# Optimization experiments

Hardware: AMD Instinct MI355X
Metric: run time of the kernel (lower is better)

## Reference

```python
import jax, jax.numpy as jnp
import numpy as np

NUM_HEADS = 8
NUM_LAYERS = 4
TOKEN_AMOUNT = 16
TOKEN_SIZE = 256
D_MODEL = 512
D_FF = 2048


def _layernorm(x, g, b, eps=1e-6):
    m = jnp.mean(x, axis=-1, keepdims=True)
    v = jnp.mean((x - m) ** 2, axis=-1, keepdims=True)
    return (x - m) / jnp.sqrt(v + eps) * g + b


def _mha(xq, xkv, W, b, mask, H):
    # W: [4, d, d] (q,k,v,o), b: [4, d]
    B, Tq, d = xq.shape
    Tk = xkv.shape[1]
    dh = d // H
    q = (xq @ W[0] + b[0]).reshape(B, Tq, H, dh).transpose(0, 2, 1, 3)
    k = (xkv @ W[1] + b[1]).reshape(B, Tk, H, dh).transpose(0, 2, 1, 3)
    v = (xkv @ W[2] + b[2]).reshape(B, Tk, H, dh).transpose(0, 2, 1, 3)
    logits = jnp.einsum('bhqd,bhkd->bhqk', q, k) / jnp.sqrt(jnp.float32(dh))
    if mask is not None:
        logits = logits - mask * jnp.finfo(jnp.float32).max
    w = jax.nn.softmax(logits, axis=-1)
    o = jnp.einsum('bhqk,bhkd->bhqd', w, v).transpose(0, 2, 1, 3).reshape(B, Tq, d)
    return o @ W[3] + b[3]


def _pos_enc(T, d):
    i = jnp.arange(d)
    factors = 1.0 / jnp.power(10000.0, (2.0 * (i // 2)).astype(jnp.float32) / d)
    ang = jnp.arange(T, dtype=jnp.float32)[:, None] * factors  # [T, d]
    return jnp.where(i % 2 == 0, jnp.sin(ang), jnp.cos(ang))


def setup_inputs() -> dict:
    key = jax.random.key(0)
    ks = jax.random.split(key, 8)
    B, Lenc, F = 16, 2048, 128
    d, dff, L, TS = D_MODEL, D_FF, NUM_LAYERS, TOKEN_SIZE
    s = 0.02
    return {
        'encoder_output': jax.random.normal(ks[0], (B, Lenc, d), jnp.float32),
        'encoder_input': jax.random.normal(ks[1], (B, Lenc, F), jnp.float32),
        'emb_W': jax.random.normal(ks[2], (TS, d), jnp.float32) * s,
        'emb_b': jnp.zeros((d,), jnp.float32),
        'out_W': jax.random.normal(ks[3], (d, TS), jnp.float32) * s,
        'out_b': jnp.zeros((TS,), jnp.float32),
        'self_W': jax.random.normal(ks[4], (L, 4, d, d), jnp.float32) * s,
        'self_b': jnp.zeros((L, 4, d), jnp.float32),
        'cross_W': jax.random.normal(ks[5], (L, 4, d, d), jnp.float32) * s,
        'cross_b': jnp.zeros((L, 4, d), jnp.float32),
        'ffn_W1': jax.random.normal(ks[6], (L, d, dff), jnp.float32) * s,
        'ffn_b1': jnp.zeros((L, dff), jnp.float32),
        'ffn_W2': jax.random.normal(ks[7], (L, dff, d), jnp.float32) * s,
        'ffn_b2': jnp.zeros((L, d), jnp.float32),
        'ln_g': jnp.ones((L, 3, d), jnp.float32),
        'ln_b': jnp.zeros((L, 3, d), jnp.float32),
    }


def reference(encoder_output, encoder_input, emb_W, emb_b, out_W, out_b,
              self_W, self_b, cross_W, cross_b,
              ffn_W1, ffn_b1, ffn_W2, ffn_b2, ln_g, ln_b):
    B = encoder_output.shape[0]
    d = emb_W.shape[1]
    H = NUM_HEADS
    # padding mask from encoder_input (mask_zero_inputs=True)
    pad_mask = jnp.min((encoder_input == 0).astype(jnp.float32), axis=2)[:, None, None, :]
    tokens = jnp.ones((B, 1, TOKEN_SIZE), dtype=jnp.float32)
    for _ in range(TOKEN_AMOUNT):
        T = tokens.shape[1]
        look_ahead = 1.0 - jnp.tril(jnp.ones((T, T), dtype=jnp.float32))
        tok_pad = jnp.min((tokens == 0).astype(jnp.float32), axis=2)[:, None, None, :]
        la_mask = jnp.maximum(tok_pad, look_ahead)
        x = (tokens @ emb_W + emb_b) * jnp.sqrt(jnp.float32(d)) + _pos_enc(T, d)
        for l in range(NUM_LAYERS):
            a = _mha(x, x, self_W[l], self_b[l], la_mask, H)
            x = _layernorm(x + a, ln_g[l, 0], ln_b[l, 0])
            c = _mha(x, encoder_output, cross_W[l], cross_b[l], pad_mask, H)
            x = _layernorm(x + c, ln_g[l, 1], ln_b[l, 1])
            f = jax.nn.relu(x @ ffn_W1[l] + ffn_b1[l]) @ ffn_W2[l] + ffn_b2[l]
            x = _layernorm(x + f, ln_g[l, 2], ln_b[l, 2])
        next_token = (x @ out_W + out_b)[:, -1:, :]
        tokens = jnp.concatenate([tokens, next_token], axis=1)
    return tokens[:, 1:, :]
```

## Files before the change

### kernel.cpp

```cpp
#include <hip/hip_runtime.h>


typedef unsigned short ushort_t;
typedef __attribute__((ext_vector_type(4))) float f32x4;
typedef __attribute__((ext_vector_type(8))) unsigned short us8;
typedef __attribute__((ext_vector_type(4))) unsigned short us4;

#define NB 256
#define NTHR 1024

__device__ __forceinline__ float bf2f(ushort_t u) {
    union { unsigned int i; float f; } v; v.i = ((unsigned int)u) << 16; return v.f;
}
__device__ __forceinline__ ushort_t f2bf(float f) {
    union { unsigned int i; float f; } v; v.f = f;
    return (ushort_t)((v.i + 0x7FFF + ((v.i >> 16) & 1)) >> 16);
}
__device__ __forceinline__ f32x4 b2f4(us4 w) {
    return (f32x4){bf2f(w[0]), bf2f(w[1]), bf2f(w[2]), bf2f(w[3])};
}
__device__ __forceinline__ float wave_sum(float v) {
    #pragma unroll
    for (int m = 32; m; m >>= 1) v += __shfl_xor(v, m);
    return v;
}
__device__ __forceinline__ float wave_max(float v) {
    #pragma unroll
    for (int m = 32; m; m >>= 1) v = fmaxf(v, __shfl_xor(v, m));
    return v;
}

union U64C { unsigned long long u; float2 f; us4 s4; };
__device__ __forceinline__ float clf(const float* p) {
    return __hip_atomic_load(p, __ATOMIC_RELAXED, __HIP_MEMORY_SCOPE_AGENT);
}
__device__ __forceinline__ void csf(float* p, float v) {
    __hip_atomic_store(p, v, __ATOMIC_RELAXED, __HIP_MEMORY_SCOPE_AGENT);
}
__device__ __forceinline__ float2 clf2(const float* p) {
    U64C c; c.u = __hip_atomic_load((unsigned long long*)p, __ATOMIC_RELAXED,
                                    __HIP_MEMORY_SCOPE_AGENT);
    return c.f;
}
__device__ __forceinline__ void csf2(float* p, float x, float y) {
    U64C c; c.f.x = x; c.f.y = y;
    __hip_atomic_store((unsigned long long*)p, c.u, __ATOMIC_RELAXED,
                       __HIP_MEMORY_SCOPE_AGENT);
}
__device__ __forceinline__ void csu4(ushort_t* p, us4 v) {
    U64C c; c.s4 = v;
    __hip_atomic_store((unsigned long long*)p, c.u, __ATOMIC_RELAXED,
                       __HIP_MEMORY_SCOPE_AGENT);
}

__device__ __forceinline__ void gbar(unsigned* bar, int g) {
    __syncthreads();
    if (threadIdx.x == 0) {
        unsigned* cnt = bar + g * 32;
        unsigned* rel = bar + 512 + g * 32;
        unsigned a = __hip_atomic_fetch_add(cnt, 1u, __ATOMIC_RELAXED,
                                            __HIP_MEMORY_SCOPE_AGENT);
        unsigned e = (a >> 4) + 1u;
        if ((a & 15u) == 15u) {
            __hip_atomic_store(rel, e, __ATOMIC_RELAXED, __HIP_MEMORY_SCOPE_AGENT);
        } else {
            while ((int)(__hip_atomic_load(rel, __ATOMIC_RELAXED,
                                           __HIP_MEMORY_SCOPE_AGENT) - e) < 0)
                __builtin_amdgcn_s_sleep(1);
        }
    }
    __syncthreads();
}
__device__ __forceinline__ void gbar_all(unsigned* bar) {
    __syncthreads();
    if (threadIdx.x == 0) {
        unsigned* cnt = bar + 1024;
        unsigned* rel = bar + 1056;
        unsigned a = __hip_atomic_fetch_add(cnt, 1u, __ATOMIC_RELAXED,
                                            __HIP_MEMORY_SCOPE_AGENT);
        unsigned e = (a >> 8) + 1u;
        if ((a & 255u) == 255u) {
            __hip_atomic_store(rel, e, __ATOMIC_RELAXED, __HIP_MEMORY_SCOPE_AGENT);
        } else {
            while ((int)(__hip_atomic_load(rel, __ATOMIC_RELAXED,
                                           __HIP_MEMORY_SCOPE_AGENT) - e) < 0)
                __builtin_amdgcn_s_sleep(1);
        }
    }
    __syncthreads();
}

__device__ __forceinline__ void ln512b(const float* __restrict__ row,
                                       const float* __restrict__ g,
                                       const float* __restrict__ be,
                                       int use_ln, float* dst, float* red) {
    int tid = threadIdx.x;
    float a = (tid < 512) ? clf(row + tid) : 0.f;
    if (use_ln) {
        float s = a, s2 = a * a;
        #pragma unroll
        for (int m = 32; m; m >>= 1) {
            s  += __shfl_xor(s, m);
            s2 += __shfl_xor(s2, m);
        }
        if ((tid & 63) == 0) { red[tid >> 6] = s; red[16 + (tid >> 6)] = s2; }
        __syncthreads();
        float ts = 0.f, ts2 = 0.f;
        #pragma unroll
        for (int i = 0; i < 8; i++) { ts += red[i]; ts2 += red[16 + i]; }
        float mu = ts * (1.f / 512.f);
        float var = ts2 * (1.f / 512.f) - mu * mu;
        float rstd = rsqrtf(var + 1e-6f);
        if (tid < 512) dst[tid] = (a - mu) * rstd * g[tid] + be[tid];
    } else {
        if (tid < 512) dst[tid] = a;
    }
    __syncthreads();
}

template<int NCQ, int K>
__device__ __forceinline__ void gemv_allf(const float* xs, const float* __restrict__ W,
                                          int ldw, int col0, float* part) {
    constexpr int S = 1024 / NCQ;
    constexpr int KS = K / S;
    int tid = threadIdx.x;
    int cq = tid & (NCQ - 1), ks = tid / NCQ;
    const float* Wp = W + (size_t)(ks * KS) * ldw + col0 + cq * 4;
    const float* xp = xs + ks * KS;
    f32x4 acc = {0.f, 0.f, 0.f, 0.f};
    #pragma unroll
    for (int r = 0; r < KS; r++)
        acc += xp[r] * *(const f32x4*)(Wp + (size_t)r * ldw);
    #pragma unroll
    for (int m = NCQ; m < 64; m <<= 1) {
        acc[0] += __shfl_xor(acc[0], m);
        acc[1] += __shfl_xor(acc[1], m);
        acc[2] += __shfl_xor(acc[2], m);
        acc[3] += __shfl_xor(acc[3], m);
    }
    int wave = tid >> 6, lane = tid & 63;
    if (lane < NCQ) *(f32x4*)(part + (wave * NCQ + lane) * 4) = acc;
    __syncthreads();
}

template<int NCQ, int K>
__device__ __forceinline__ void gemv_allb(const float* xs, const ushort_t* __restrict__ W,
                                          int ldw, int col0, float* part) {
    constexpr int S = 1024 / NCQ;
    constexpr int KS = K / S;
    int tid = threadIdx.x;
    int cq = tid & (NCQ - 1), ks = tid / NCQ;
    const ushort_t* Wp = W + (size_t)(ks * KS) * ldw + col0 + cq * 4;
    const float* xp = xs + ks * KS;
    f32x4 acc = {0.f, 0.f, 0.f, 0.f};
    #pragma unroll
    for (int r = 0; r < KS; r++)
        acc += xp[r] * b2f4(*(const us4*)(Wp + (size_t)r * ldw));
    #pragma unroll
    for (int m = NCQ; m < 64; m <<= 1) {
        acc[0] += __shfl_xor(acc[0], m);
        acc[1] += __shfl_xor(acc[1], m);
        acc[2] += __shfl_xor(acc[2], m);
        acc[3] += __shfl_xor(acc[3], m);
    }
    int wave = tid >> 6, lane = tid & 63;
    if (lane < NCQ) *(f32x4*)(part + (wave * NCQ + lane) * 4) = acc;
    __syncthreads();
}
template<int NCQ>
__device__ __forceinline__ float gemv_allr(const float* part) {
    float a = 0.f;
    #pragma unroll
    for (int w = 0; w < 16; w++) a += part[w * NCQ * 4 + threadIdx.x];
    return a;
}

struct Args {
    const float *enc, *encIn, *embW, *embB, *outW, *outB;
    const float *selfW, *selfB, *crossW, *crossB;
    const float *fW1, *fb1, *fW2, *fb2, *lng, *lnb;
    float* out;
    unsigned* bar;
    float *x0, *qbuf, *y1, *y2, *y3, *attnb;
    float *lny1, *lny2, *qt, *Pm2, *Ps2, *Pz, *tmpb, *selfK, *selfV;
    ushort_t *selfWb, *crossWb, *fW1b, *fW2b;
};


__global__ __launch_bounds__(NTHR, 4) void k_mega(Args A) {
    __shared__ ushort_t encL[128 * 520];
    __shared__ float padL[128];
    __shared__ float sm[6400];
    const int bid = blockIdx.x, tid = threadIdx.x;
    const int b = bid >> 4, r = bid & 15;
    unsigned* bar = A.bar;

    {
        const float* ep = A.enc + ((size_t)b * 2048 + r * 128) * 512;
        #pragma unroll 4
        for (int it = 0; it < 16; it++) {
            int idx = tid + it * 1024;
            int key = idx >> 7;
            int d = (idx & 127) * 4;
            float4 v = *(const float4*)(ep + (size_t)key * 512 + d);
            us4 o; o[0] = f2bf(v.x); o[1] = f2bf(v.y); o[2] = f2bf(v.z); o[3] = f2bf(v.w);
            *(us4*)(encL + key * 520 + d) = o;
        }
        int key = tid >> 3, sub = tid & 7;
        const float* p = A.encIn + ((size_t)b * 2048 + r * 128 + key) * 128 + sub * 16;
        int ok = 1;
        #pragma unroll
        for (int j = 0; j < 4; j++) {
            float4 v = *(const float4*)(p + j * 4);
            ok &= (v.x == 0.f) & (v.y == 0.f) & (v.z == 0.f) & (v.w == 0.f);
        }
        ok &= __shfl_xor(ok, 1); ok &= __shfl_xor(ok, 2); ok &= __shfl_xor(ok, 4);
        if (sub == 0) padL[key] = ok ? 1.f : 0.f;
        const float* srcs[4] = {A.selfW, A.crossW, A.fW1, A.fW2};
        ushort_t* dsts[4] = {A.selfWb, A.crossWb, A.fW1b, A.fW2b};
        #pragma unroll
        for (int a = 0; a < 4; a++) {
            const float* s = srcs[a];
            ushort_t* d = dsts[a];
            #pragma unroll
            for (int it = 0; it < 4; it++) {
                size_t i = (size_t)bid * 16384 + (size_t)(it * 1024 + tid) * 4;
                float4 v = *(const float4*)(s + i);
                us4 o; o[0] = f2bf(v.x); o[1] = f2bf(v.y); o[2] = f2bf(v.z); o[3] = f2bf(v.w);
                csu4(d + i, o);
            }
        }
    }
    gbar_all(bar);

    for (int t = 0; t < 16; t++) {
        {
            float* tok = sm;
            float* part = sm + 256;
            if (tid < 256)
                tok[tid] = (t == 0) ? 1.f
                         : clf(A.out + (size_t)b * 4096 + (t - 1) * 256 + tid);
            __syncthreads();
            gemv_allf<8, 256>(tok, A.embW, 512, r * 32, part);
            if (tid < 32) {
                float acc = gemv_allr<8>(part);
                int col = r * 32 + tid;
                float expo = (2.0f * (float)(col >> 1)) * (1.f / 512.f);
                float ang = (float)t * powf(10000.0f, -expo);
                float pv = (col & 1) ? cosf(ang) : sinf(ang);
                csf(A.x0 + (size_t)b * 512 + col,
                    (acc + A.embB[col]) * 22.627416997969522f + pv);
            }
        }
        gbar(bar, b);

        for (int l = 0; l < 4; l++) {
            const float* src = (l == 0) ? A.x0 : A.y3;
            const float* gP = (l == 0) ? nullptr : A.lng + ((l - 1) * 3 + 2) * 512;
            const float* bP = (l == 0) ? nullptr : A.lnb + ((l - 1) * 3 + 2) * 512;
            int ulnP = (l != 0);

            {
                float* xs = sm;
                float* red = sm + 512;
                float* part = sm + 1024;
                ln512b(src + (size_t)b * 512, gP, bP, ulnP, xs, red);
                int cq = tid & 7, ks = tid >> 3;
                const float* xp = xs + ks * 4;
                f32x4 a0 = {0.f,0.f,0.f,0.f}, a1 = a0, a2 = a0;
                const ushort_t* W0 = A.selfWb + ((size_t)(l * 4 + 0)) * 262144
                                   + (size_t)(ks * 4) * 512 + r * 32 + cq * 4;
                const ushort_t* W1 = W0 + 262144;
                const ushort_t* W2 = W1 + 262144;
                #pragma unroll
                for (int rr = 0; rr < 4; rr++) {
                    float x = xp[rr];
                    a0 += x * b2f4(*(const us4*)(W0 + (size_t)rr * 512));
                    a1 += x * b2f4(*(const us4*)(W1 + (size_t)rr * 512));
                    a2 += x * b2f4(*(const us4*)(W2 + (size_t)rr * 512));
                }
                #pragma unroll
                for (int m = 8; m < 64; m <<= 1) {
                    #pragma unroll
                    for (int j = 0; j < 4; j++) {
                        a0[j] += __shfl_xor(a0[j], m);
                        a1[j] += __shfl_xor(a1[j], m);
                        a2[j] += __shfl_xor(a2[j], m);
                    }
                }
                int wave = tid >> 6, lane = tid & 63;
                if (lane < 8) {
                    *(f32x4*)(part + (wave * 8 + lane) * 4) = a0;
                    *(f32x4*)(part + 512 + (wave * 8 + lane) * 4) = a1;
                    *(f32x4*)(part + 1024 + (wave * 8 + lane) * 4) = a2;
                }
                __syncthreads();
                if (tid < 96) {
                    int m = tid >> 5, j = tid & 31;
                    float a = 0.f;
                    #pragma unroll
                    for (int w = 0; w < 16; w++) a += part[m * 512 + w * 32 + j];
                    int col = r * 32 + j;
                    a += A.selfB[(l * 4 + m) * 512 + col];
                    if (m == 0) csf(A.qbuf + (size_t)b * 512 + col, a);
                    else if (m == 1)
                        csf(A.selfK + (((size_t)l * 16 + b) * 16 + t) * 512 + col, a);
                    else
                        csf(A.selfV + (((size_t)l * 16 + b) * 16 + t) * 512 + col, a);
                }
            }
            gbar(bar, b);

            {
                float* xr = sm;
                float* qs = sm + 512;
                float* as2 = sm + 1024;
                float* lg = sm + 5120;
                float* red = sm + 5248;
                float* part = sm + 5280;
                ln512b(src + (size_t)b * 512, gP, bP, ulnP, xr, red);
                if (tid < 256) {
                    float2 v = clf2(A.qbuf + (size_t)b * 512 + tid * 2);
                    qs[tid * 2] = v.x; qs[tid * 2 + 1] = v.y;
                }
                __syncthreads();
                const float* Kb = A.selfK + ((size_t)l * 16 + b) * 16 * 512;
                const float* Vb = A.selfV + ((size_t)l * 16 + b) * 16 * 512;
                {
                    int idx = tid >> 3, kp = tid & 7;
                    int h = idx >> 4, j = idx & 15;
                    if (j <= t) {
                        const float* kpp = Kb + (size_t)j * 512 + h * 64 + kp * 8;
                        const float* qp = qs + h * 64 + kp * 8;
                        float4 k0 = *(const float4*)kpp;
                        float4 k1 = *(const float4*)(kpp + 4);
                        float s = qp[0]*k0.x + qp[1]*k0.y + qp[2]*k0.z + qp[3]*k0.w
                                + qp[4]*k1.x + qp[5]*k1.y + qp[6]*k1.z + qp[7]*k1.w;
                        s += __shfl_xor(s, 1);
                        s += __shfl_xor(s, 2);
                        s += __shfl_xor(s, 4);
                        if (kp == 0) lg[h * 16 + j] = s * 0.125f;
                    }
                }
                __syncthreads();
                if (tid < 8) {
                    float m = -1e30f;
                    for (int j = 0; j <= t; j++) m = fmaxf(m, lg[tid * 16 + j]);
                    float ssum = 0.f;
                    for (int j = 0; j <= t; j++) {
                        float e = __expf(lg[tid * 16 + j] - m);
                        lg[tid * 16 + j] = e; ssum += e;
                    }
                    float inv = 1.f / ssum;
                    for (int j = 0; j <= t; j++) lg[tid * 16 + j] *= inv;
                }
                __syncthreads();
                {
                    int cq2 = tid & 127, js = tid >> 7;
                    int col0 = cq2 * 4, h = col0 >> 6;
                    f32x4 acc = {0.f, 0.f, 0.f, 0.f};
                    for (int j = js; j <= t; j += 8) {
                        float4 v = *(const float4*)(Vb + (size_t)j * 512 + col0);
                        float w = lg[h * 16 + j];
                        acc[0] += w * v.x; acc[1] += w * v.y;
                        acc[2] += w * v.z; acc[3] += w * v.w;
                    }
                    *(f32x4*)(as2 + js * 512 + col0) = acc;
                }
                __syncthreads();
                if (tid < 512) {
                    float a = 0.f;
                    #pragma unroll
                    for (int s = 0; s < 8; s++) a += as2[s * 512 + tid];
                    qs[tid] = a;
                }
                __syncthreads();
                gemv_allb<8, 512>(qs, A.selfWb + ((size_t)(l * 4 + 3)) * 262144,
                                  512, r * 32, part);
                if (tid < 32) {
                    int col = r * 32 + tid;
                    csf(A.y1 + (size_t)b * 512 + col,
                        gemv_allr<8>(part) + A.selfB[(l * 4 + 3) * 512 + col] + xr[col]);
                }
            }
            gbar(bar, b);

            {
                int h = r >> 1, half = r & 1;
                float* xsw = sm;
                float* red = sm + 512;
                float* qch = sm + 544;
                float* part = sm + 1024;
                ln512b(A.y1 + (size_t)b * 512, A.lng + (l * 3) * 512,
                       A.lnb + (l * 3) * 512, 1, xsw, red);
                if (r == 0 && tid < 512)
                    csf(A.lny1 + (size_t)b * 512 + tid, xsw[tid]);
                gemv_allb<16, 512>(xsw, A.crossWb + ((size_t)(l * 4)) * 262144,
                                   512, h * 64, part);
                if (tid < 64)
                    qch[tid] = gemv_allr<16>(part)
                             + A.crossB[(l * 4) * 512 + h * 64 + tid];
                __syncthreads();
                {
                    int D = half * 256 + (tid >> 2), q4 = tid & 3;
                    const ushort_t* wr = A.crossWb + ((size_t)(l * 4 + 1)) * 262144
                                       + (size_t)D * 512 + h * 64 + q4 * 16;
                    const float* qp = qch + q4 * 16;
                    float a = 0.f;
                    #pragma unroll
                    for (int j = 0; j < 16; j += 4) {
                        f32x4 wv = b2f4(*(const us4*)(wr + j));
                        a += qp[j]*wv[0] + qp[j+1]*wv[1] + qp[j+2]*wv[2] + qp[j+3]*wv[3];
                    }
                    a += __shfl_xor(a, 1);
                    a += __shfl_xor(a, 2);
                    if (q4 == 0)
                        csf(A.qt + ((size_t)b * 8 + h) * 512 + D, a * 0.125f);
                }
            }
            gbar(bar, b);

            {
                float* qts = sm;
                float* lge = sm + 4160;
                float* wms = sm + 5184;
                float* wss = sm + 5200;
                #pragma unroll
                for (int it = 0; it < 2; it++) {
                    int p = (tid + it * 1024) * 2;
                    float2 v = clf2(A.qt + (size_t)b * 4096 + p);
                    int row = p >> 9, d = p & 511;
                    qts[row * 520 + d] = v.x;
                    qts[row * 520 + d + 1] = v.y;
                }
                __syncthreads();
                #pragma unroll
                for (int it = 0; it < 4; it++) {
                    int key = it * 32 + (tid >> 5);
                    int hh = (tid >> 2) & 7, pq = tid & 3;
                    const ushort_t* er = encL + key * 520;
                    const float* q = qts + hh * 520;
                    float a0 = 0.f, a1 = 0.f;
                    #pragma unroll
                    for (int ch = 0; ch < 16; ch++) {
                        int c8 = (pq + ch * 4) * 8;
                        us8 ev8 = *(const us8*)(er + c8);
                        const float* qp = q + c8;
                        a0 += bf2f(ev8[0])*qp[0] + bf2f(ev8[1])*qp[1]
                            + bf2f(ev8[2])*qp[2] + bf2f(ev8[3])*qp[3];
                        a1 += bf2f(ev8[4])*qp[4] + bf2f(ev8[5])*qp[5]
                            + bf2f(ev8[6])*qp[6] + bf2f(ev8[7])*qp[7];
                    }
                    float acc = a0 + a1;
                    acc += __shfl_xor(acc, 1);
                    acc += __shfl_xor(acc, 2);
                    if (pq == 0)
                        lge[hh * 128 + key] = (padL[key] != 0.f) ? -2e30f : acc;
                }
                __syncthreads();
                {
                    int hh = tid >> 7, k = tid & 127;
                    float lv = lge[hh * 128 + k];
                    float mv = wave_max(lv);
                    if ((tid & 63) == 0) wms[tid >> 6] = mv;
                    __syncthreads();
                    float m = fmaxf(wms[hh * 2], wms[hh * 2 + 1]);
                    float ev = __expf(lv - m);
                    float sv = wave_sum(ev);
                    if ((tid & 63) == 0) wss[tid >> 6] = sv;
                    lge[hh * 128 + k] = ev;
                    __syncthreads();
                    if (tid < 8) {
                        int bc = b * 16 + r;
                        csf(A.Pm2 + bc * 8 + tid, fmaxf(wms[tid * 2], wms[tid * 2 + 1]));
                        csf(A.Ps2 + bc * 8 + tid, wss[tid * 2] + wss[tid * 2 + 1]);
                    }
                }
                __syncthreads();
                {
                    int hz = tid >> 7, ii = tid & 127;
                    f32x4 z = {0.f, 0.f, 0.f, 0.f};
                    const ushort_t* ep2 = encL + ii * 4;
                    const float* le = lge + hz * 128;
                    #pragma unroll 4
                    for (int k = 0; k < 128; k++) {
                        float ev = le[k];
                        us4 e4 = *(const us4*)(ep2 + k * 520);
                        z[0] += ev * bf2f(e4[0]); z[1] += ev * bf2f(e4[1]);
                        z[2] += ev * bf2f(e4[2]); z[3] += ev * bf2f(e4[3]);
                    }
                    float* dst = A.Pz + ((size_t)((b * 16 + r) * 8 + hz)) * 512 + ii * 4;
                    csf2(dst, z[0], z[1]);
                    csf2(dst + 2, z[2], z[3]);
                }
            }
            gbar(bar, b);

            {
                int h = r >> 1, half = r & 1;
                float* zs = sm;
                float* zs2 = sm + 512;
                float* ecs = sm + 2560;
                float* part = sm + 2624;
                if (tid < 16) {
                    float mcv = clf(A.Pm2 + (b * 16 + tid) * 8 + h);
                    float mm = mcv;
                    mm = fmaxf(mm, __shfl_xor(mm, 1));
                    mm = fmaxf(mm, __shfl_xor(mm, 2));
                    mm = fmaxf(mm, __shfl_xor(mm, 4));
                    mm = fmaxf(mm, __shfl_xor(mm, 8));
                    float ec = __expf(mcv - mm);
                    float sv = ec * clf(A.Ps2 + (b * 16 + tid) * 8 + h);
                    sv += __shfl_xor(sv, 1); sv += __shfl_xor(sv, 2);
                    sv += __shfl_xor(sv, 4); sv += __shfl_xor(sv, 8);
                    ecs[tid] = ec;
                    if (tid == 0) ecs[16] = 1.f / sv;
                }
                __syncthreads();
                {
                    int cp = (tid & 255) * 2, qtr = tid >> 8;
                    float a0 = 0.f, a1 = 0.f;
                    #pragma unroll
                    for (int j = 0; j < 4; j++) {
                        int cc = qtr * 4 + j;
                        float2 v = clf2(A.Pz + ((size_t)(b * 16 + cc) * 8 + h) * 512 + cp);
                        a0 += ecs[cc] * v.x; a1 += ecs[cc] * v.y;
                    }
                    zs2[qtr * 512 + cp] = a0;
                    zs2[qtr * 512 + cp + 1] = a1;
                }
                __syncthreads();
                if (tid < 512)
                    zs[tid] = (zs2[tid] + zs2[512 + tid] + zs2[1024 + tid]
                             + zs2[1536 + tid]) * ecs[16];
                __syncthreads();
                gemv_allb<8, 512>(zs, A.crossWb + ((size_t)(l * 4 + 2)) * 262144,
                                  512, h * 64 + half * 32, part);
                if (tid < 32) {
                    int col = h * 64 + half * 32 + tid;
                    csf(A.attnb + (size_t)b * 512 + col,
                        gemv_allr<8>(part) + A.crossB[(l * 4 + 2) * 512 + col]);
                }
            }
            gbar(bar, b);

            {
                float* xa = sm;
                float* part = sm + 512;
                if (tid < 256) {
                    float2 v = clf2(A.attnb + (size_t)b * 512 + tid * 2);
                    xa[tid * 2] = v.x; xa[tid * 2 + 1] = v.y;
                }
                __syncthreads();
                gemv_allb<8, 512>(xa, A.crossWb + ((size_t)(l * 4 + 3)) * 262144,
                                  512, r * 32, part);
                if (tid < 32) {
                    int col = r * 32 + tid;
                    csf(A.y2 + (size_t)b * 512 + col,
                        gemv_allr<8>(part) + A.crossB[(l * 4 + 3) * 512 + col]
                        + clf(A.lny1 + (size_t)b * 512 + col));
                }
            }
            gbar(bar, b);

            {
                float* xsw = sm;
                float* red = sm + 512;
                float* part = sm + 1024;
                ln512b(A.y2 + (size_t)b * 512, A.lng + (l * 3 + 1) * 512,
                       A.lnb + (l * 3 + 1) * 512, 1, xsw, red);
                if (r == 0 && tid < 512)
                    csf(A.lny2 + (size_t)b * 512 + tid, xsw[tid]);
                gemv_allb<32, 512>(xsw, A.fW1b + (size_t)l * 512 * 2048,
                                   2048, r * 128, part);
                if (tid < 128) {
                    int col = r * 128 + tid;
                    csf(A.tmpb + (size_t)b * 2048 + col,
                        fmaxf(gemv_allr<32>(part) + A.fb1[l * 2048 + col], 0.f));
                }
            }
            gbar(bar, b);

            {
                float* ts = sm;
                float* part = sm + 2048;
                {
                    float2 v = clf2(A.tmpb + (size_t)b * 2048 + tid * 2);
                    ts[tid * 2] = v.x; ts[tid * 2 + 1] = v.y;
                }
                __syncthreads();
                gemv_allb<8, 2048>(ts, A.fW2b + (size_t)l * 2048 * 512,
                                   512, r * 32, part);
                if (tid < 32) {
                    int col = r * 32 + tid;
                    csf(A.y3 + (size_t)b * 512 + col,
                        gemv_allr<8>(part) + A.fb2[l * 512 + col]
                        + clf(A.lny2 + (size_t)b * 512 + col));
                }
            }
            gbar(bar, b);
        }

        {
            float* xsw = sm;
            float* red = sm + 512;
            float* part = sm + 1024;
            ln512b(A.y3 + (size_t)b * 512, A.lng + 11 * 512, A.lnb + 11 * 512,
                   1, xsw, red);
            gemv_allf<4, 512>(xsw, A.outW, 256, r * 16, part);
            if (tid < 16) {
                int col = r * 16 + tid;
                csf(A.out + (size_t)b * 4096 + t * 256 + col,
                    gemv_allr<4>(part) + A.outB[col]);
            }
        }
        gbar(bar, b);
    }
}


extern "C" void kernel_launch(void* const* d_in, const int* in_sizes, int n_in,
                              void* d_out, int out_size, void* d_ws, size_t ws_size,
                              hipStream_t stream) {
    Args A;
    A.enc    = (const float*)d_in[0];
    A.encIn  = (const float*)d_in[1];
    A.embW   = (const float*)d_in[2];
    A.embB   = (const float*)d_in[3];
    A.outW   = (const float*)d_in[4];
    A.outB   = (const float*)d_in[5];
    A.selfW  = (const float*)d_in[6];
    A.selfB  = (const float*)d_in[7];
    A.crossW = (const float*)d_in[8];
    A.crossB = (const float*)d_in[9];
    A.fW1    = (const float*)d_in[10];
    A.fb1    = (const float*)d_in[11];
    A.fW2    = (const float*)d_in[12];
    A.fb2    = (const float*)d_in[13];
    A.lng    = (const float*)d_in[14];
    A.lnb    = (const float*)d_in[15];
    A.out    = (float*)d_out;

    char* ws = (char*)d_ws;
    size_t off = 0;
    auto alloc = [&](size_t bytes) -> char* {
        char* p = ws + off;
        off = (off + bytes + 255) & ~(size_t)255;
        return p;
    };
    char* barrier = alloc(8192);
    A.bar = (unsigned*)barrier;
    A.x0    = (float*)alloc(16 * 512 * 4);
    A.qbuf  = (float*)alloc(16 * 512 * 4);
    A.y1    = (float*)alloc(16 * 512 * 4);
    A.y2    = (float*)alloc(16 * 512 * 4);
    A.y3    = (float*)alloc(16 * 512 * 4);
    A.attnb = (float*)alloc(16 * 512 * 4);
    A.lny1  = (float*)alloc(16 * 512 * 4);
    A.lny2  = (float*)alloc(16 * 512 * 4);
    A.qt    = (float*)alloc((size_t)16 * 8 * 512 * 4);
    A.Pm2   = (float*)alloc(16 * 16 * 8 * 4);
    A.Ps2   = (float*)alloc(16 * 16 * 8 * 4);
    A.Pz    = (float*)alloc((size_t)16 * 16 * 8 * 512 * 4);
    A.tmpb  = (float*)alloc((size_t)16 * 2048 * 4);
    A.selfK = (float*)alloc((size_t)4 * 16 * 16 * 512 * 4);
    A.selfV = (float*)alloc((size_t)4 * 16 * 16 * 512 * 4);
    A.selfWb  = (ushort_t*)alloc((size_t)4 * 4 * 512 * 512 * 2);
    A.crossWb = (ushort_t*)alloc((size_t)4 * 4 * 512 * 512 * 2);
    A.fW1b    = (ushort_t*)alloc((size_t)4 * 512 * 2048 * 2);
    A.fW2b    = (ushort_t*)alloc((size_t)4 * 2048 * 512 * 2);
    if (off > ws_size) return;

    hipMemsetAsync(barrier, 0, 8192, stream);
    k_mega<<<dim3(NB), dim3(NTHR), 0, stream>>>(A);
}
```

Baseline: 4.884 ms.

## Fold embedding into output projection and fuse cross-attn V and O weights

Precomputes Mo = outW·embW (scaled) so the next token's embedding comes straight from the final layernormed state. This removes the separate embedding phase and one grid barrier per token. When workspace allows, it also precomputes per-head products of Wv and Wo (Wvc, 4096x512 per layer) plus a folded bias. The cross-attention value and output projections then become a single GEMV over the concatenated per-head contexts, which drops one barrier per layer. The costs are a larger prologue, more weight bytes read per step (the 4096-row GEMV reads eight times as many weight bytes as one 512x512 projection), and extra bf16 rounding of the precomposed matrices.

```diff
diff --git a/kernel.cpp b/kernel.cpp
--- a/kernel.cpp
+++ b/kernel.cpp
@@ -50,6 +50,11 @@
 __device__ __forceinline__ void csu4(ushort_t* p, us4 v) {
     U64C c; c.s4 = v;
     __hip_atomic_store((unsigned long long*)p, c.u, __ATOMIC_RELAXED,
+                       __HIP_MEMORY_SCOPE_AGENT);
+}
+__device__ __forceinline__ void csu2(ushort_t* p, float a0, float a1) {
+    unsigned u = (unsigned)f2bf(a0) | ((unsigned)f2bf(a1) << 16);
+    __hip_atomic_store((unsigned*)p, u, __ATOMIC_RELAXED,
                        __HIP_MEMORY_SCOPE_AGENT);
 }
 
@@ -184,6 +189,9 @@
     float *x0, *qbuf, *y1, *y2, *y3, *attnb;
     float *lny1, *lny2, *qt, *Pm2, *Ps2, *Pz, *tmpb, *selfK, *selfV;
     ushort_t *selfWb, *crossWb, *fW1b, *fW2b;
+    ushort_t *Mo, *Wvc;
+    float *cvec, *bco2;
+    int fused;
 };
 
 
@@ -230,30 +238,70 @@
                 csu4(d + i, o);
             }
         }
+        if (tid < 512) {
+            int row = bid * 2 + (tid >> 8);
+            int cp = tid & 255;
+            float a0 = 0.f, a1 = 0.f;
+            const float* op = A.outW + (size_t)row * 256;
+            for (int v = 0; v < 256; v++) {
+                float w = op[v];
+                a0 += w * A.embW[(size_t)v * 512 + cp * 2];
+                a1 += w * A.embW[(size_t)v * 512 + cp * 2 + 1];
+            }
+            csu2(A.Mo + (size_t)row * 512 + cp * 2,
+                 a0 * 22.627416997969522f, a1 * 22.627416997969522f);
+        }
+        if (bid < 8) {
+            int idx = bid * 1024 + tid;
+            int col = idx & 511;
+            float acc = 0.f;
+            for (int v = 0; v < 256; v++) acc += A.embW[(size_t)v * 512 + col];
+            csf(A.x0 + idx, (acc + A.embB[col]) * 22.627416997969522f
+                            + ((col & 1) ? 1.f : 0.f));
+        }
+        if (bid == 8 && tid < 512) {
+            float acc = 0.f;
+            for (int v = 0; v < 256; v++)
+                acc += A.outB[v] * A.embW[(size_t)v * 512 + tid];
+            csf(A.cvec + tid, (acc + A.embB[tid]) * 22.627416997969522f);
+        }
+        if (bid >= 12 && bid < 16 && tid < 512) {
+            int l = bid - 12;
+            const float* bv = A.crossB + (l * 4 + 2) * 512;
+            const float* Wco = A.crossW + ((size_t)(l * 4 + 3)) * 262144;
+            float acc = 0.f;
+            for (int d = 0; d < 512; d++)
+                acc += bv[d] * Wco[(size_t)d * 512 + tid];
+            csf(A.bco2 + l * 512 + tid, acc + A.crossB[(l * 4 + 3) * 512 + tid]);
+        }
+        if (A.fused) {
+            int base = bid * 64;
+            int act = ((tid >> 8) & 1) == 0;
+            int cp = tid & 255;
+            for (int it = 0; it < 32; it++) {
+                int rid = base + it * 2 + (tid >> 9);
+                int l = rid >> 12, rem = rid & 4095;
+                int h = rem >> 9, D = rem & 511;
+                if (act) {
+                    const float* Wv = A.crossW + ((size_t)(l * 4 + 2)) * 262144
+                                    + (size_t)D * 512 + h * 64;
+                    const float* Wco = A.crossW + ((size_t)(l * 4 + 3)) * 262144
+                                     + (size_t)(h * 64) * 512 + cp * 2;
+                    float a0 = 0.f, a1 = 0.f;
+                    #pragma unroll 8
+                    for (int dv = 0; dv < 64; dv++) {
+                        float w = Wv[dv];
+                        a0 += w * Wco[(size_t)dv * 512];
+                        a1 += w * Wco[(size_t)dv * 512 + 1];
+                    }
+                    csu2(A.Wvc + (size_t)rid * 512 + cp * 2, a0, a1);
+                }
+            }
+        }
     }
     gbar_all(bar);
 
     for (int t = 0; t < 16; t++) {
-        {
-            float* tok = sm;
-            float* part = sm + 256;
-            if (tid < 256)
-                tok[tid] = (t == 0) ? 1.f
-                         : clf(A.out + (size_t)b * 4096 + (t - 1) * 256 + tid);
-            __syncthreads();
-            gemv_allf<8, 256>(tok, A.embW, 512, r * 32, part);
-            if (tid < 32) {
-                float acc = gemv_allr<8>(part);
-                int col = r * 32 + tid;
-                float expo = (2.0f * (float)(col >> 1)) * (1.f / 512.f);
-                float ang = (float)t * powf(10000.0f, -expo);
-                float pv = (col & 1) ? cosf(ang) : sinf(ang);
-                csf(A.x0 + (size_t)b * 512 + col,
-                    (acc + A.embB[col]) * 22.627416997969522f + pv);
-            }
-        }
-        gbar(bar, b);
-
         for (int l = 0; l < 4; l++) {
             const float* src = (l == 0) ? A.x0 : A.y3;
             const float* gP = (l == 0) ? nullptr : A.lng + ((l - 1) * 3 + 2) * 512;
@@ -496,72 +544,115 @@
             }
             gbar(bar, b);
 
-            {
-                int h = r >> 1, half = r & 1;
-                float* zs = sm;
-                float* zs2 = sm + 512;
-                float* ecs = sm + 2560;
-                float* part = sm + 2624;
-                if (tid < 16) {
-                    float mcv = clf(A.Pm2 + (b * 16 + tid) * 8 + h);
+            if (A.fused) {
+                float* zcat = sm;
+                float* ecs  = sm + 4096;
+                float* inv  = sm + 4224;
+                float* part = sm + 4352;
+                if (tid < 128) {
+                    int h = tid >> 4, cc = tid & 15;
+                    float mcv = clf(A.Pm2 + (b * 16 + cc) * 8 + h);
                     float mm = mcv;
                     mm = fmaxf(mm, __shfl_xor(mm, 1));
                     mm = fmaxf(mm, __shfl_xor(mm, 2));
                     mm = fmaxf(mm, __shfl_xor(mm, 4));
                     mm = fmaxf(mm, __shfl_xor(mm, 8));
                     float ec = __expf(mcv - mm);
-                    float sv = ec * clf(A.Ps2 + (b * 16 + tid) * 8 + h);
+                    float sv = ec * clf(A.Ps2 + (b * 16 + cc) * 8 + h);
                     sv += __shfl_xor(sv, 1); sv += __shfl_xor(sv, 2);
                     sv += __shfl_xor(sv, 4); sv += __shfl_xor(sv, 8);
-                    ecs[tid] = ec;
-                    if (tid == 0) ecs[16] = 1.f / sv;
-                }
-                __syncthreads();
-                {
-                    int cp = (tid & 255) * 2, qtr = tid >> 8;
-                    float a0 = 0.f, a1 = 0.f;
+                    ecs[h * 16 + cc] = ec;
+                    if (cc == 0) inv[h] = 1.f / sv;
+                }
+                __syncthreads();
+                #pragma unroll
+                for (int it = 0; it < 4; it++) {
+                    int idx = tid + it * 1024;
+                    int h = idx >> 9, D = idx & 511;
+                    float a = 0.f;
                     #pragma unroll
-                    for (int j = 0; j < 4; j++) {
-                        int cc = qtr * 4 + j;
-                        float2 v = clf2(A.Pz + ((size_t)(b * 16 + cc) * 8 + h) * 512 + cp);
-                        a0 += ecs[cc] * v.x; a1 += ecs[cc] * v.y;
-                    }
-                    zs2[qtr * 512 + cp] = a0;
-                    zs2[qtr * 512 + cp + 1] = a1;
-                }
-                __syncthreads();
-                if (tid < 512)
-                    zs[tid] = (zs2[tid] + zs2[512 + tid] + zs2[1024 + tid]
-                             + zs2[1536 + tid]) * ecs[16];
-                __syncthreads();
-                gemv_allb<8, 512>(zs, A.crossWb + ((size_t)(l * 4 + 2)) * 262144,
-                                  512, h * 64 + half * 32, part);
-                if (tid < 32) {
-                    int col = h * 64 + half * 32 + tid;
-                    csf(A.attnb + (size_t)b * 512 + col,
-                        gemv_allr<8>(part) + A.crossB[(l * 4 + 2) * 512 + col]);
-                }
-            }
-            gbar(bar, b);
-
-            {
-                float* xa = sm;
-                float* part = sm + 512;
-                if (tid < 256) {
-                    float2 v = clf2(A.attnb + (size_t)b * 512 + tid * 2);
-                    xa[tid * 2] = v.x; xa[tid * 2 + 1] = v.y;
-                }
-                __syncthreads();
-                gemv_allb<8, 512>(xa, A.crossWb + ((size_t)(l * 4 + 3)) * 262144,
-                                  512, r * 32, part);
+                    for (int cc = 0; cc < 16; cc++)
+                        a += ecs[h * 16 + cc]
+                           * clf(A.Pz + ((size_t)(b * 16 + cc) * 8 + h) * 512 + D);
+                    zcat[idx] = a * inv[h];
+                }
+                __syncthreads();
+                gemv_allb<8, 4096>(zcat, A.Wvc + (size_t)l * 4096 * 512,
+                                   512, r * 32, part);
                 if (tid < 32) {
                     int col = r * 32 + tid;
                     csf(A.y2 + (size_t)b * 512 + col,
-                        gemv_allr<8>(part) + A.crossB[(l * 4 + 3) * 512 + col]
+                        gemv_allr<8>(part) + A.bco2[l * 512 + col]
                         + clf(A.lny1 + (size_t)b * 512 + col));
                 }
-            }
-            gbar(bar, b);
+                gbar(bar, b);
+            } else {
+                {
+                    int h = r >> 1, half = r & 1;
+                    float* zs = sm;
+                    float* zs2 = sm + 512;
+                    float* ecs = sm + 2560;
+                    float* part = sm + 2624;
+                    if (tid < 16) {
+                        float mcv = clf(A.Pm2 + (b * 16 + tid) * 8 + h);
+                        float mm = mcv;
+                        mm = fmaxf(mm, __shfl_xor(mm, 1));
+                        mm = fmaxf(mm, __shfl_xor(mm, 2));
+                        mm = fmaxf(mm, __shfl_xor(mm, 4));
+                        mm = fmaxf(mm, __shfl_xor(mm, 8));
+                        float ec = __expf(mcv - mm);
+                        float sv = ec * clf(A.Ps2 + (b * 16 + tid) * 8 + h);
+                        sv += __shfl_xor(sv, 1); sv += __shfl_xor(sv, 2);
+                        sv += __shfl_xor(sv, 4); sv += __shfl_xor(sv, 8);
+                        ecs[tid] = ec;
+                        if (tid == 0) ecs[16] = 1.f / sv;
+                    }
+                    __syncthreads();
+                    {
+                        int cp = (tid & 255) * 2, qtr = tid >> 8;
+                        float a0 = 0.f, a1 = 0.f;
+                        #pragma unroll
+                        for (int j = 0; j < 4; j++) {
+                            int cc = qtr * 4 + j;
+                            float2 v = clf2(A.Pz + ((size_t)(b * 16 + cc) * 8 + h) * 512 + cp);
+                            a0 += ecs[cc] * v.x; a1 += ecs[cc] * v.y;
+                        }
+                        zs2[qtr * 512 + cp] = a0;
+                        zs2[qtr * 512 + cp + 1] = a1;
+                    }
+                    __syncthreads();
+                    if (tid < 512)
+                        zs[tid] = (zs2[tid] + zs2[512 + tid] + zs2[1024 + tid]
+                                 + zs2[1536 + tid]) * ecs[16];
+                    __syncthreads();
+                    gemv_allb<8, 512>(zs, A.crossWb + ((size_t)(l * 4 + 2)) * 262144,
+                                      512, h * 64 + half * 32, part);
+                    if (tid < 32) {
+                        int col = h * 64 + half * 32 + tid;
+                        csf(A.attnb + (size_t)b * 512 + col,
+                            gemv_allr<8>(part) + A.crossB[(l * 4 + 2) * 512 + col]);
+                    }
+                }
+                gbar(bar, b);
+                {
+                    float* xa = sm;
+                    float* part = sm + 512;
+                    if (tid < 256) {
+                        float2 v = clf2(A.attnb + (size_t)b * 512 + tid * 2);
+                        xa[tid * 2] = v.x; xa[tid * 2 + 1] = v.y;
+                    }
+                    __syncthreads();
+                    gemv_allb<8, 512>(xa, A.crossWb + ((size_t)(l * 4 + 3)) * 262144,
+                                      512, r * 32, part);
+                    if (tid < 32) {
+                        int col = r * 32 + tid;
+                        csf(A.y2 + (size_t)b * 512 + col,
+                            gemv_allr<8>(part) + A.crossB[(l * 4 + 3) * 512 + col]
+                            + clf(A.lny1 + (size_t)b * 512 + col));
+                    }
+                }
+                gbar(bar, b);
+            }
 
             {
                 float* xsw = sm;
@@ -612,6 +703,18 @@
                 int col = r * 16 + tid;
                 csf(A.out + (size_t)b * 4096 + t * 256 + col,
                     gemv_allr<4>(part) + A.outB[col]);
+            }
+            __syncthreads();
+            if (t < 15) {
+                gemv_allb<8, 512>(xsw, A.Mo, 512, r * 32, part);
+                if (tid < 32) {
+                    int col = r * 32 + tid;
+                    float expo = (2.0f * (float)(col >> 1)) * (1.f / 512.f);
+                    float ang = (float)(t + 1) * powf(10000.0f, -expo);
+                    float pv = (col & 1) ? cosf(ang) : sinf(ang);
+                    csf(A.x0 + (size_t)b * 512 + col,
+                        gemv_allr<8>(part) + A.cvec[col] + pv);
+                }
             }
         }
         gbar(bar, b);
@@ -669,7 +772,17 @@
     A.crossWb = (ushort_t*)alloc((size_t)4 * 4 * 512 * 512 * 2);
     A.fW1b    = (ushort_t*)alloc((size_t)4 * 512 * 2048 * 2);
     A.fW2b    = (ushort_t*)alloc((size_t)4 * 2048 * 512 * 2);
-    if (off > ws_size) return;
+    A.Mo      = (ushort_t*)alloc((size_t)512 * 512 * 2);
+    A.cvec    = (float*)alloc(512 * 4);
+    A.bco2    = (float*)alloc(4 * 512 * 4);
+    size_t base_need = off;
+    A.Wvc = nullptr;
+    A.fused = 0;
+    if (off + (size_t)4 * 4096 * 512 * 2 + 256 <= ws_size) {
+        A.Wvc = (ushort_t*)alloc((size_t)4 * 4096 * 512 * 2);
+        A.fused = 1;
+    }
+    if (base_need > ws_size) return;
 
     hipMemsetAsync(barrier, 0, 8192, stream);
     k_mega<<<dim3(NB), dim3(NTHR), 0, stream>>>(A);
```

After: 7.552 ms. +54.6%, slower.
